# Kernel tuning notes

Hardware: AMD Instinct MI355X
Metric: run time of the kernel (lower is better)

The kernel has to match this reference:

```python
import jax, jax.numpy as jnp
import numpy as np

WH, WW = 16, 16          # window_size
C = 384                  # in_channel
H = 12                   # num_heads
HD = C // H              # head_dim = 32
B = 256                  # num_windows * batch
N = WH * WW              # tokens per window = 256
CPB_HID = 512


def _build_buffers():
    # relative_coords_table: [1, 2*WH-1, 2*WW-1, 2], log-spaced coords (pretrain_window_size = [0,0])
    rch = np.arange(-(WH - 1), WH, dtype=np.float32)
    rcw = np.arange(-(WW - 1), WW, dtype=np.float32)
    table = np.stack(np.meshgrid(rch, rcw, indexing='ij'), axis=-1)[None]  # [1,2WH-1,2WW-1,2]
    table[..., 0] /= (WH - 1)
    table[..., 1] /= (WW - 1)
    table = np.sign(table) * np.log2(np.abs(table) + 1.0) / np.log2(8)
    # relative_position_index: [N, N] int indices into flattened table
    ch = np.arange(WH)
    cw = np.arange(WW)
    coords = np.stack(np.meshgrid(ch, cw, indexing='ij'))      # [2, WH, WW]
    cf = coords.reshape(2, -1)                                  # [2, N]
    rel = cf[:, :, None] - cf[:, None, :]                       # [2, N, N]
    rel = rel.transpose(1, 2, 0).astype(np.int64)               # [N, N, 2]
    rel[..., 0] += WH - 1
    rel[..., 1] += WW - 1
    rel[..., 0] *= 2 * WW - 1
    rpi = rel.sum(-1)                                           # [N, N]
    return jnp.asarray(table, jnp.float32), jnp.asarray(rpi, jnp.int32)


def setup_inputs() -> dict:
    key = jax.random.key(0)
    ks = jax.random.split(key, 9)
    table, rpi = _build_buffers()
    return {
        'x': jax.random.normal(ks[0], (B, N, C), jnp.float32),
        'qkv_w': jax.random.normal(ks[1], (3 * C, C), jnp.float32) * 0.02,
        'q_bias': jnp.zeros((C,), jnp.float32),
        'v_bias': jnp.zeros((C,), jnp.float32),
        'logit_scale': jnp.log(10.0 * jnp.ones((H, 1, 1), jnp.float32)),
        'cpb_w1': jax.random.normal(ks[2], (CPB_HID, 2), jnp.float32) * 0.02,
        'cpb_b1': jnp.zeros((CPB_HID,), jnp.float32),
        'cpb_w2': jax.random.normal(ks[3], (H, CPB_HID), jnp.float32) * 0.02,
        'proj_w': jax.random.normal(ks[4], (C, C), jnp.float32) * 0.02,
        'proj_b': jnp.zeros((C,), jnp.float32),
        'rel_coords_table': table,
        'rel_pos_index': rpi,
    }


def reference(x, qkv_w, q_bias, v_bias, logit_scale, cpb_w1, cpb_b1, cpb_w2,
              proj_w, proj_b, rel_coords_table, rel_pos_index):
    b, n, c = x.shape
    h, hd = H, c // H
    # qkv with q/v bias, zero k bias
    bias = jnp.concatenate([q_bias, jnp.zeros_like(v_bias), v_bias])
    qkv = x @ qkv_w.T + bias                                   # [B,N,3C]
    qkv = qkv.reshape(b, n, 3, h, hd).transpose(2, 0, 3, 1, 4)  # [3,B,H,N,hd]
    q, k, v = qkv[0], qkv[1], qkv[2]
    # cosine attention: L2-normalize q, k (F.normalize with eps=1e-12)
    qn = q / jnp.maximum(jnp.linalg.norm(q, axis=-1, keepdims=True), 1e-12)
    kn = k / jnp.maximum(jnp.linalg.norm(k, axis=-1, keepdims=True), 1e-12)
    attn = jnp.einsum('bhnd,bhmd->bhnm', qn, kn)               # [B,H,N,N]
    # learnable per-head logit scale, clamped at log(1/0.01)
    scale = jnp.exp(jnp.minimum(logit_scale, jnp.log(100.0)))  # [H,1,1]
    attn = attn * scale
    # continuous relative position bias MLP: 2 -> 512 -> H
    hid = jax.nn.relu(rel_coords_table @ cpb_w1.T + cpb_b1)    # [1,2WH-1,2WW-1,512]
    bias_table = (hid @ cpb_w2.T).reshape(-1, h)               # [(2WH-1)*(2WW-1), H]
    rpb = bias_table[rel_pos_index.reshape(-1)].reshape(n, n, h).transpose(2, 0, 1)
    rpb = 16.0 * jax.nn.sigmoid(rpb)                           # [H,N,N]
    attn = jax.nn.softmax(attn + rpb, axis=-1)
    out = jnp.einsum('bhnm,bhmd->bhnd', attn, v)               # [B,H,N,hd]
    out = out.transpose(0, 2, 1, 3).reshape(b, n, c)
    return out @ proj_w.T + proj_b
```

## Files before the change

### kernel.cpp

```cpp
#include <hip/hip_runtime.h>

typedef unsigned int uint;
typedef unsigned short ushort_t;
typedef ushort_t ushort8 __attribute__((ext_vector_type(8)));
typedef ushort_t ushort4v __attribute__((ext_vector_type(4)));
typedef short short8 __attribute__((ext_vector_type(8)));
typedef float floatx4 __attribute__((ext_vector_type(4)));
typedef uint uint2v __attribute__((ext_vector_type(2)));
typedef uint uint4v __attribute__((ext_vector_type(4)));

#define WSQ 25165824L
#define NH  12
#define NT  256
#define HD  32

__device__ __forceinline__ float bf2f(ushort_t u) {
    uint x = ((uint)u) << 16;
    return __builtin_bit_cast(float, x);
}
__device__ __forceinline__ ushort_t f2bf(float f) {
    uint u = __builtin_bit_cast(uint, f);
    uint lsb = (u >> 16) & 1u;
    return (ushort_t)((u + 0x7FFFu + lsb) >> 16);
}
__device__ __forceinline__ uint cvt_pk_bf16(float lo, float hi) {
    uint r;
    asm("v_cvt_pk_bf16_f32 %0, %1, %2" : "=v"(r) : "v"(lo), "v"(hi));
    return r;
}
__device__ __forceinline__ float exp2_fast(float x) {
    float r;
    asm("v_exp_f32 %0, %1" : "=v"(r) : "v"(x));
    return r;
}
__device__ __forceinline__ void permlane32_swap(uint& a, uint& b) {
    uint2v r = __builtin_amdgcn_permlane32_swap(a, b, false, false);
    a = r[0]; b = r[1];
}
__device__ __forceinline__ void permlane16_swap(uint& a, uint& b) {
    uint2v r = __builtin_amdgcn_permlane16_swap(a, b, false, false);
    a = r[0]; b = r[1];
}
__device__ __forceinline__ float ld1(const void* p, long i, int f) {
    return f ? ((const float*)p)[i] : bf2f(((const ushort_t*)p)[i]);
}

__global__ void detect_kernel(const ushort_t* __restrict__ x, int* __restrict__ flag) {
    int t = threadIdx.x;
    uint u = x[2 * t];
    int e = (u >> 7) & 0xFF;
    int weird = (e > 147 || e < 107) ? 1 : 0;
    unsigned long long b = __ballot(weird);
    if (t == 0) *flag = (__popcll(b) > 19) ? 1 : 0;
}

__global__ __launch_bounds__(256) void cvt_kernel(
    const void* __restrict__ src, ushort_t* __restrict__ dst,
    const int* __restrict__ fl, long n8)
{
    long i = (long)blockIdx.x * 256 + threadIdx.x;
    if (i >= n8) return;
    if (*fl) {
        const floatx4* s = (const floatx4*)((const float*)src + i * 8);
        floatx4 a = s[0], b = s[1];
        ushort8 o;
        for (int j = 0; j < 4; ++j) { o[j] = f2bf(a[j]); o[4 + j] = f2bf(b[j]); }
        *(ushort8*)(dst + i * 8) = o;
    } else {
        *(ushort8*)(dst + i * 8) = *(const ushort8*)((const ushort_t*)src + i * 8);
    }
}

__global__ __launch_bounds__(512) void cpb_kernel(
    const void* __restrict__ tab, const void* __restrict__ w1,
    const void* __restrict__ b1, const void* __restrict__ w2,
    const int* __restrict__ fl, float* __restrict__ bt)
{
    __shared__ float hid[512];
    const int f = *fl;
    int p = blockIdx.x, j = threadIdx.x;
    float c0 = ld1(tab, p * 2 + 0, f);
    float c1 = ld1(tab, p * 2 + 1, f);
    float v = ld1(w1, j * 2 + 0, f) * c0 + ld1(w1, j * 2 + 1, f) * c1 + ld1(b1, j, f);
    hid[j] = fmaxf(v, 0.0f);
    __syncthreads();
    if (j < NH) {
        float s = 0.0f;
        for (int i = 0; i < 512; ++i) s += hid[i] * ld1(w2, (long)j * 512 + i, f);
        bt[p * NH + j] = s;
    }
}

__global__ __launch_bounds__(256) void rpb_kernel(
    const int* __restrict__ rpi, const float* __restrict__ bt,
    const void* __restrict__ ls, const int* __restrict__ fl,
    float* __restrict__ rpb)
{
    int idx = blockIdx.x * 256 + threadIdx.x;
    int h = idx >> 16, ij = idx & 65535;
    float x = bt[rpi[ij] * NH + h];
    float scale = __expf(fminf(ld1(ls, h, *fl), 4.6051702f)) * 1.44269504f;
    float bound = fminf(scale, 40.0f) * 1.02f + 23.1f;
    rpb[idx] = 1.44269504f * 16.0f / (1.0f + __expf(-x)) - bound;
}

template <int MODE>
__global__ __launch_bounds__(256) void gemm_bt(
    const ushort_t* __restrict__ A, const ushort_t* __restrict__ Bw,
    const void* __restrict__ bias0, const void* __restrict__ bias2,
    void* __restrict__ Cout, const int* __restrict__ fl)
{
    const int K = 384;
    const int NBX = (MODE == 0) ? 9 : 3;
    const int CHUNK = NBX * 512 / 8;
    __shared__ ushort_t As[128 * 72];
    __shared__ ushort_t Bs[128 * 72];
    const int f = *fl;
    const int tid = threadIdx.x;
    const int w = tid >> 6, lane = tid & 63, l15 = lane & 15, quad = lane >> 4;
    const int bid = blockIdx.x;
    const int wg = (bid & 7) * CHUNK + (bid >> 3);
    const int m0 = (wg / NBX) * 128, n0 = (wg % NBX) * 128;
    const int rw = (w >> 1) * 64, cw = (w & 1) * 64;
    const int lr = tid >> 3, lc = (tid & 7) * 8;

    floatx4 acc[4][4] = {};
    ushort8 pa[4], pb[4];

    for (int i = 0; i < 4; ++i) {
        int r = lr + i * 32;
        if (MODE == 0) {
            pa[i] = *(const ushort8*)&A[(long)(m0 + r) * K + lc];
        } else {
            int m = m0 + r, kc = lc;
            long ad = ((long)(m >> 8) * 12 + (kc >> 5)) * 8192 + (m & 255) * 32 + (kc & 31);
            pa[i] = *(const ushort8*)&A[ad];
        }
        pb[i] = *(const ushort8*)&Bw[(long)(n0 + r) * K + lc];
    }

    for (int kt = 0; kt < K; kt += 64) {
        for (int i = 0; i < 4; ++i) {
            int r = lr + i * 32;
            *(ushort8*)&As[r * 72 + lc] = pa[i];
            *(ushort8*)&Bs[r * 72 + lc] = pb[i];
        }
        __syncthreads();
        if (kt + 64 < K) {
            for (int i = 0; i < 4; ++i) {
                int r = lr + i * 32;
                if (MODE == 0) {
                    pa[i] = *(const ushort8*)&A[(long)(m0 + r) * K + kt + 64 + lc];
                } else {
                    int m = m0 + r, kc = kt + 64 + lc;
                    long ad = ((long)(m >> 8) * 12 + (kc >> 5)) * 8192 + (m & 255) * 32 + (kc & 31);
                    pa[i] = *(const ushort8*)&A[ad];
                }
                pb[i] = *(const ushort8*)&Bw[(long)(n0 + r) * K + kt + 64 + lc];
            }
        }
        for (int ks = 0; ks < 64; ks += 32) {
            short8 af[4], bfr[4];
            for (int mt = 0; mt < 4; ++mt)
                af[mt] = *(short8*)&As[(rw + mt * 16 + l15) * 72 + ks + quad * 8];
            for (int nt = 0; nt < 4; ++nt)
                bfr[nt] = *(short8*)&Bs[(cw + nt * 16 + l15) * 72 + ks + quad * 8];
            for (int mt = 0; mt < 4; ++mt)
                for (int nt = 0; nt < 4; ++nt)
                    acc[mt][nt] = __builtin_amdgcn_mfma_f32_16x16x32_bf16(
                        af[mt], bfr[nt], acc[mt][nt], 0, 0, 0);
        }
        __syncthreads();
    }

    for (int mt = 0; mt < 4; ++mt) {
        for (int nt = 0; nt < 4; ++nt) {
            int c = n0 + cw + nt * 16 + l15;
            if (MODE == 0) {
                int which = c / 384, cc = c % 384;
                float bias = (which == 0) ? ld1(bias0, cc, f)
                           : (which == 2) ? ld1(bias2, cc, f) : 0.0f;
                int hh = cc >> 5, dd = cc & 31;
                for (int r = 0; r < 4; ++r) {
                    int m = m0 + rw + mt * 16 + quad * 4 + r;
                    int b = m >> 8, ntok = m & 255;
                    long dst = (long)which * WSQ +
                               (((long)(b * NH + hh) * NT + ntok) * HD + dd);
                    ((ushort_t*)Cout)[dst] = f2bf(acc[mt][nt][r] + bias);
                }
            } else {
                float bias = ld1(bias0, c, f);
                for (int r = 0; r < 4; ++r) {
                    int m = m0 + rw + mt * 16 + quad * 4 + r;
                    float v = acc[mt][nt][r] + bias;
                    long o = (long)m * 384 + c;
                    if (f) ((float*)Cout)[o] = v;
                    else   ((ushort_t*)Cout)[o] = f2bf(v);
                }
            }
        }
    }
}

__global__ __launch_bounds__(256, 4) void attn_kernel(
    ushort_t* __restrict__ qkv, const void* __restrict__ ls,
    const float* __restrict__ rpb, const int* __restrict__ fl)
{
    __shared__ __attribute__((aligned(16))) ushort_t ks[256 * 40];
    __shared__ __attribute__((aligned(16))) ushort_t vts[32 * 264];

    const int f = *fl;
    const int bid = blockIdx.x;
    const int xcd = bid & 7, local = bid >> 3;
    const int h = local >> 5, bwin = (xcd << 5) + (local & 31);
    const int bh = bwin * NH + h;
    ushort_t* qp = qkv + (long)bh * NT * HD;
    const ushort_t* kp = qp + WSQ;
    const ushort_t* vp = qp + 2 * WSQ;
    const int tid = threadIdx.x;
    const float scale = __expf(fminf(ld1(ls, h, f), 4.6051702f)) * 1.44269504f;

    {
        const int t = tid;
        ushort8 kv[4];
        #pragma unroll
        for (int i = 0; i < 4; ++i) kv[i] = *(const ushort8*)&kp[t * HD + i * 8];
        float fv[32]; float ss = 0.0f;
        #pragma unroll
        for (int i = 0; i < 4; ++i)
            #pragma unroll
            for (int j = 0; j < 8; ++j) {
                float v = bf2f(kv[i][j]); fv[i * 8 + j] = v; ss += v * v;
            }
        float rn = 1.0f / fmaxf(sqrtf(ss), 1e-12f);
        #pragma unroll
        for (int i = 0; i < 4; ++i) {
            uint4v o;
            #pragma unroll
            for (int j = 0; j < 4; ++j)
                o[j] = cvt_pk_bf16(fv[i * 8 + 2 * j] * rn, fv[i * 8 + 2 * j + 1] * rn);
            *(uint4v*)&ks[t * 40 + i * 8] = o;
        }
        ushort8 vv[4];
        #pragma unroll
        for (int i = 0; i < 4; ++i) vv[i] = *(const ushort8*)&vp[t * HD + i * 8];
        #pragma unroll
        for (int i = 0; i < 4; ++i)
            #pragma unroll
            for (int j = 0; j < 8; ++j) vts[(i * 8 + j) * 264 + t] = vv[i][j];
    }
    __syncthreads();

    const int w = tid >> 6, lane = tid & 63, l15 = lane & 15, quad = lane >> 4;

    if (scale <= 40.0f) {
      for (int c = 0; c < 4; ++c) {
        const int mloc = w * 64 + c * 16;

        ushort8 qv = *(const ushort8*)&qp[(mloc + l15) * HD + quad * 8];
        float qf[8]; float ss = 0.0f;
        #pragma unroll
        for (int j = 0; j < 8; ++j) { qf[j] = bf2f(qv[j]); ss += qf[j] * qf[j]; }
        ss += __shfl_xor(ss, 16, 64);
        ss += __shfl_xor(ss, 32, 64);
        float rn = 1.0f / fmaxf(sqrtf(ss), 1e-12f);
        uint4v qa;
        #pragma unroll
        for (int j = 0; j < 4; ++j)
            qa[j] = cvt_pk_bf16(qf[2 * j] * rn, qf[2 * j + 1] * rn);
        short8 aq = __builtin_bit_cast(short8, qa);

        floatx4 accS[16];
        #pragma unroll
        for (int t = 0; t < 16; ++t) {
            short8 bk = *(short8*)&ks[(t * 16 + l15) * 40 + quad * 8];
            floatx4 z = {};
            accS[t] = __builtin_amdgcn_mfma_f32_16x16x32_bf16(bk, aq, z, 0, 0, 0);
        }

        const float* rp = rpb + ((long)h * NT + mloc + l15) * NT;
        const floatx4* rp4 = (const floatx4*)rp;

        float s4[4] = {0.f, 0.f, 0.f, 0.f};
        floatx4 accO[2] = {};
        floatx4 rb0 = rp4[quad], rb1 = rp4[4 + quad];
        #pragma unroll
        for (int kk = 0; kk < 8; ++kk) {
            short8 vf0 = *(short8*)&vts[l15 * 264 + kk * 32 + quad * 8];
            short8 vf1 = *(short8*)&vts[(16 + l15) * 264 + kk * 32 + quad * 8];
            floatx4 nb0 = rb0, nb1 = rb1;
            if (kk < 7) { nb0 = rp4[8 * (kk + 1) + quad]; nb1 = rp4[8 * (kk + 1) + 4 + quad]; }
            const int t0 = 2 * kk, t1 = 2 * kk + 1;
            float a0 = exp2_fast(fmaf(accS[t0][0], scale, rb0[0]));
            float a1 = exp2_fast(fmaf(accS[t0][1], scale, rb0[1]));
            float a2 = exp2_fast(fmaf(accS[t0][2], scale, rb0[2]));
            float a3 = exp2_fast(fmaf(accS[t0][3], scale, rb0[3]));
            float e0 = exp2_fast(fmaf(accS[t1][0], scale, rb1[0]));
            float e1 = exp2_fast(fmaf(accS[t1][1], scale, rb1[1]));
            float e2 = exp2_fast(fmaf(accS[t1][2], scale, rb1[2]));
            float e3 = exp2_fast(fmaf(accS[t1][3], scale, rb1[3]));
            s4[0] += a0 + e0; s4[1] += a1 + e1;
            s4[2] += a2 + e2; s4[3] += a3 + e3;
            uint A0 = cvt_pk_bf16(a0, a1), A1 = cvt_pk_bf16(a2, a3);
            uint B0 = cvt_pk_bf16(e0, e1), B1 = cvt_pk_bf16(e2, e3);
            permlane32_swap(A0, B0); permlane16_swap(A0, B0);
            permlane32_swap(A1, B1); permlane16_swap(A1, B1);
            uint4v pw; pw[0] = A0; pw[1] = A1; pw[2] = B0; pw[3] = B1;
            short8 pf = __builtin_bit_cast(short8, pw);
            accO[0] = __builtin_amdgcn_mfma_f32_16x16x32_bf16(pf, vf0, accO[0], 0, 0, 0);
            accO[1] = __builtin_amdgcn_mfma_f32_16x16x32_bf16(pf, vf1, accO[1], 0, 0, 0);
            rb0 = nb0; rb1 = nb1;
        }

        float rsum = (s4[0] + s4[1]) + (s4[2] + s4[3]);
        rsum += __shfl_xor(rsum, 16, 64);
        rsum += __shfl_xor(rsum, 32, 64);
        float rinv = 1.0f / rsum;
        float ri[4];
        #pragma unroll
        for (int r = 0; r < 4; ++r) ri[r] = __shfl(rinv, quad * 4 + r, 64);

        #pragma unroll
        for (int tn = 0; tn < 2; ++tn)
            #pragma unroll
            for (int r = 0; r < 4; r += 2) {
                uint pk = cvt_pk_bf16(accO[tn][r] * ri[r], accO[tn][r + 1] * ri[r + 1]);
                int n = mloc + quad * 4 + r;
                qp[n * HD + tn * 16 + l15] = (ushort_t)pk;
                qp[(n + 1) * HD + tn * 16 + l15] = (ushort_t)(pk >> 16);
            }
      }
    } else {
      for (int c = 0; c < 4; ++c) {
        const int mloc = w * 64 + c * 16;

        ushort8 qv = *(const ushort8*)&qp[(mloc + l15) * HD + quad * 8];
        float qf[8]; float ss = 0.0f;
        #pragma unroll
        for (int j = 0; j < 8; ++j) { qf[j] = bf2f(qv[j]); ss += qf[j] * qf[j]; }
        ss += __shfl_xor(ss, 16, 64);
        ss += __shfl_xor(ss, 32, 64);
        float rn = 1.0f / fmaxf(sqrtf(ss), 1e-12f);
        uint4v qa;
        #pragma unroll
        for (int j = 0; j < 4; ++j)
            qa[j] = cvt_pk_bf16(qf[2 * j] * rn, qf[2 * j + 1] * rn);
        short8 aq = __builtin_bit_cast(short8, qa);

        floatx4 accS[16];
        #pragma unroll
        for (int t = 0; t < 16; ++t) {
            short8 bk = *(short8*)&ks[(t * 16 + l15) * 40 + quad * 8];
            floatx4 z = {};
            accS[t] = __builtin_amdgcn_mfma_f32_16x16x32_bf16(bk, aq, z, 0, 0, 0);
        }

        const float* rp = rpb + ((long)h * NT + mloc + l15) * NT;
        float m4[4] = {-3e38f, -3e38f, -3e38f, -3e38f};
        #pragma unroll
        for (int t = 0; t < 16; ++t) {
            floatx4 rb = *(const floatx4*)&rp[t * 16 + quad * 4];
            float v0 = fmaf(accS[t][0], scale, rb[0]);
            float v1 = fmaf(accS[t][1], scale, rb[1]);
            float v2 = fmaf(accS[t][2], scale, rb[2]);
            float v3 = fmaf(accS[t][3], scale, rb[3]);
            accS[t][0] = v0; accS[t][1] = v1; accS[t][2] = v2; accS[t][3] = v3;
            m4[t & 3] = fmaxf(m4[t & 3], fmaxf(fmaxf(v0, v1), fmaxf(v2, v3)));
        }
        float rmax = fmaxf(fmaxf(m4[0], m4[1]), fmaxf(m4[2], m4[3]));
        rmax = fmaxf(rmax, __shfl_xor(rmax, 16, 64));
        rmax = fmaxf(rmax, __shfl_xor(rmax, 32, 64));

        float s4[4] = {0.f, 0.f, 0.f, 0.f};
        floatx4 accO[2] = {};
        #pragma unroll
        for (int kk = 0; kk < 8; ++kk) {
            short8 vf0 = *(short8*)&vts[l15 * 264 + kk * 32 + quad * 8];
            short8 vf1 = *(short8*)&vts[(16 + l15) * 264 + kk * 32 + quad * 8];
            const int t0 = 2 * kk, t1 = 2 * kk + 1;
            float a0 = exp2_fast(accS[t0][0] - rmax);
            float a1 = exp2_fast(accS[t0][1] - rmax);
            float a2 = exp2_fast(accS[t0][2] - rmax);
            float a3 = exp2_fast(accS[t0][3] - rmax);
            float e0 = exp2_fast(accS[t1][0] - rmax);
            float e1 = exp2_fast(accS[t1][1] - rmax);
            float e2 = exp2_fast(accS[t1][2] - rmax);
            float e3 = exp2_fast(accS[t1][3] - rmax);
            s4[0] += a0 + e0; s4[1] += a1 + e1;
            s4[2] += a2 + e2; s4[3] += a3 + e3;
            uint A0 = cvt_pk_bf16(a0, a1), A1 = cvt_pk_bf16(a2, a3);
            uint B0 = cvt_pk_bf16(e0, e1), B1 = cvt_pk_bf16(e2, e3);
            permlane32_swap(A0, B0); permlane16_swap(A0, B0);
            permlane32_swap(A1, B1); permlane16_swap(A1, B1);
            uint4v pw; pw[0] = A0; pw[1] = A1; pw[2] = B0; pw[3] = B1;
            short8 pf = __builtin_bit_cast(short8, pw);
            accO[0] = __builtin_amdgcn_mfma_f32_16x16x32_bf16(pf, vf0, accO[0], 0, 0, 0);
            accO[1] = __builtin_amdgcn_mfma_f32_16x16x32_bf16(pf, vf1, accO[1], 0, 0, 0);
        }

        float rsum = (s4[0] + s4[1]) + (s4[2] + s4[3]);
        rsum += __shfl_xor(rsum, 16, 64);
        rsum += __shfl_xor(rsum, 32, 64);
        float rinv = 1.0f / rsum;
        float ri[4];
        #pragma unroll
        for (int r = 0; r < 4; ++r) ri[r] = __shfl(rinv, quad * 4 + r, 64);

        #pragma unroll
        for (int tn = 0; tn < 2; ++tn)
            #pragma unroll
            for (int r = 0; r < 4; r += 2) {
                uint pk = cvt_pk_bf16(accO[tn][r] * ri[r], accO[tn][r + 1] * ri[r + 1]);
                int n = mloc + quad * 4 + r;
                qp[n * HD + tn * 16 + l15] = (ushort_t)pk;
                qp[(n + 1) * HD + tn * 16 + l15] = (ushort_t)(pk >> 16);
            }
      }
    }
}

extern "C" void kernel_launch(void* const* d_in, const int* in_sizes, int n_in,
                              void* d_out, int out_size, void* d_ws, size_t ws_size,
                              hipStream_t stream)
{
    const void* x      = d_in[0];
    const void* qkv_w  = d_in[1];
    const void* q_bias = d_in[2];
    const void* v_bias = d_in[3];
    const void* lscale = d_in[4];
    const void* cpb_w1 = d_in[5];
    const void* cpb_b1 = d_in[6];
    const void* cpb_w2 = d_in[7];
    const void* proj_w = d_in[8];
    const void* proj_b = d_in[9];
    const void* rct    = d_in[10];
    const int*  rpi    = (const int*)d_in[11];

    char* ws = (char*)d_ws;
    ushort_t* qkv_ws  = (ushort_t*)ws;
    float*    bt      = (float*)(ws + 150994944L);
    float*    rpb     = (float*)(ws + 151060480L);
    int*      flag    = (int*)(ws + 154206208L);
    ushort_t* wqkv_b  = (ushort_t*)(ws + 154206464L);
    ushort_t* wproj_b = (ushort_t*)(ws + 155091200L);
    ushort_t* xb      = (ushort_t*)d_out;

    detect_kernel<<<1, 64, 0, stream>>>((const ushort_t*)x, flag);
    cvt_kernel<<<12288, 256, 0, stream>>>(x, xb, flag, 3145728L);
    cvt_kernel<<<216, 256, 0, stream>>>(qkv_w, wqkv_b, flag, 55296L);
    cvt_kernel<<<72, 256, 0, stream>>>(proj_w, wproj_b, flag, 18432L);
    cpb_kernel<<<961, 512, 0, stream>>>(rct, cpb_w1, cpb_b1, cpb_w2, flag, bt);
    rpb_kernel<<<3072, 256, 0, stream>>>(rpi, bt, lscale, flag, rpb);
    gemm_bt<0><<<4608, 256, 0, stream>>>(xb, wqkv_b, q_bias, v_bias, qkv_ws, flag);
    attn_kernel<<<3072, 256, 0, stream>>>(qkv_ws, lscale, rpb, flag);
    gemm_bt<1><<<1536, 256, 0, stream>>>(qkv_ws, wproj_b, proj_b, nullptr, d_out, flag);
}
```

Measured before the change: 468.8 us.

## Fuse fp32-to-bf16 input conversion into GEMM loads and raise MFMA wave priority

```diff
diff --git a/kernel.cpp b/kernel.cpp
--- a/kernel.cpp
+++ b/kernel.cpp
@@ -44,6 +44,17 @@
 __device__ __forceinline__ float ld1(const void* p, long i, int f) {
     return f ? ((const float*)p)[i] : bf2f(((const ushort_t*)p)[i]);
 }
+__device__ __forceinline__ ushort8 ld_bf8(const void* p, long idx, int f) {
+    if (f) {
+        const floatx4* s = (const floatx4*)((const float*)p + idx);
+        floatx4 a = s[0], b = s[1];
+        uint4v u;
+        u[0] = cvt_pk_bf16(a[0], a[1]); u[1] = cvt_pk_bf16(a[2], a[3]);
+        u[2] = cvt_pk_bf16(b[0], b[1]); u[3] = cvt_pk_bf16(b[2], b[3]);
+        return __builtin_bit_cast(ushort8, u);
+    }
+    return *(const ushort8*)((const ushort_t*)p + idx);
+}
 
 __global__ void detect_kernel(const ushort_t* __restrict__ x, int* __restrict__ flag) {
     int t = threadIdx.x;
@@ -52,23 +63,6 @@
     int weird = (e > 147 || e < 107) ? 1 : 0;
     unsigned long long b = __ballot(weird);
     if (t == 0) *flag = (__popcll(b) > 19) ? 1 : 0;
-}
-
-__global__ __launch_bounds__(256) void cvt_kernel(
-    const void* __restrict__ src, ushort_t* __restrict__ dst,
-    const int* __restrict__ fl, long n8)
-{
-    long i = (long)blockIdx.x * 256 + threadIdx.x;
-    if (i >= n8) return;
-    if (*fl) {
-        const floatx4* s = (const floatx4*)((const float*)src + i * 8);
-        floatx4 a = s[0], b = s[1];
-        ushort8 o;
-        for (int j = 0; j < 4; ++j) { o[j] = f2bf(a[j]); o[4 + j] = f2bf(b[j]); }
-        *(ushort8*)(dst + i * 8) = o;
-    } else {
-        *(ushort8*)(dst + i * 8) = *(const ushort8*)((const ushort_t*)src + i * 8);
-    }
 }
 
 __global__ __launch_bounds__(512) void cpb_kernel(
@@ -106,7 +100,7 @@
 
 template <int MODE>
 __global__ __launch_bounds__(256) void gemm_bt(
-    const ushort_t* __restrict__ A, const ushort_t* __restrict__ Bw,
+    const void* __restrict__ A, const void* __restrict__ Bw,
     const void* __restrict__ bias0, const void* __restrict__ bias2,
     void* __restrict__ Cout, const int* __restrict__ fl)
 {
@@ -130,13 +124,13 @@
     for (int i = 0; i < 4; ++i) {
         int r = lr + i * 32;
         if (MODE == 0) {
-            pa[i] = *(const ushort8*)&A[(long)(m0 + r) * K + lc];
+            pa[i] = ld_bf8(A, (long)(m0 + r) * K + lc, f);
         } else {
             int m = m0 + r, kc = lc;
             long ad = ((long)(m >> 8) * 12 + (kc >> 5)) * 8192 + (m & 255) * 32 + (kc & 31);
-            pa[i] = *(const ushort8*)&A[ad];
-        }
-        pb[i] = *(const ushort8*)&Bw[(long)(n0 + r) * K + lc];
+            pa[i] = *(const ushort8*)&((const ushort_t*)A)[ad];
+        }
+        pb[i] = ld_bf8(Bw, (long)(n0 + r) * K + lc, f);
     }
 
     for (int kt = 0; kt < K; kt += 64) {
@@ -150,13 +144,13 @@
             for (int i = 0; i < 4; ++i) {
                 int r = lr + i * 32;
                 if (MODE == 0) {
-                    pa[i] = *(const ushort8*)&A[(long)(m0 + r) * K + kt + 64 + lc];
+                    pa[i] = ld_bf8(A, (long)(m0 + r) * K + kt + 64 + lc, f);
                 } else {
                     int m = m0 + r, kc = kt + 64 + lc;
                     long ad = ((long)(m >> 8) * 12 + (kc >> 5)) * 8192 + (m & 255) * 32 + (kc & 31);
-                    pa[i] = *(const ushort8*)&A[ad];
+                    pa[i] = *(const ushort8*)&((const ushort_t*)A)[ad];
                 }
-                pb[i] = *(const ushort8*)&Bw[(long)(n0 + r) * K + kt + 64 + lc];
+                pb[i] = ld_bf8(Bw, (long)(n0 + r) * K + kt + 64 + lc, f);
             }
         }
         for (int ks = 0; ks < 64; ks += 32) {
@@ -165,10 +159,12 @@
                 af[mt] = *(short8*)&As[(rw + mt * 16 + l15) * 72 + ks + quad * 8];
             for (int nt = 0; nt < 4; ++nt)
                 bfr[nt] = *(short8*)&Bs[(cw + nt * 16 + l15) * 72 + ks + quad * 8];
+            __builtin_amdgcn_s_setprio(1);
             for (int mt = 0; mt < 4; ++mt)
                 for (int nt = 0; nt < 4; ++nt)
                     acc[mt][nt] = __builtin_amdgcn_mfma_f32_16x16x32_bf16(
                         af[mt], bfr[nt], acc[mt][nt], 0, 0, 0);
+            __builtin_amdgcn_s_setprio(0);
         }
         __syncthreads();
     }
@@ -271,12 +267,14 @@
         short8 aq = __builtin_bit_cast(short8, qa);
 
         floatx4 accS[16];
+        __builtin_amdgcn_s_setprio(1);
         #pragma unroll
         for (int t = 0; t < 16; ++t) {
             short8 bk = *(short8*)&ks[(t * 16 + l15) * 40 + quad * 8];
             floatx4 z = {};
             accS[t] = __builtin_amdgcn_mfma_f32_16x16x32_bf16(bk, aq, z, 0, 0, 0);
         }
+        __builtin_amdgcn_s_setprio(0);
 
         const float* rp = rpb + ((long)h * NT + mloc + l15) * NT;
         const floatx4* rp4 = (const floatx4*)rp;
@@ -307,8 +305,10 @@
             permlane32_swap(A1, B1); permlane16_swap(A1, B1);
             uint4v pw; pw[0] = A0; pw[1] = A1; pw[2] = B0; pw[3] = B1;
             short8 pf = __builtin_bit_cast(short8, pw);
+            __builtin_amdgcn_s_setprio(1);
             accO[0] = __builtin_amdgcn_mfma_f32_16x16x32_bf16(pf, vf0, accO[0], 0, 0, 0);
             accO[1] = __builtin_amdgcn_mfma_f32_16x16x32_bf16(pf, vf1, accO[1], 0, 0, 0);
+            __builtin_amdgcn_s_setprio(0);
             rb0 = nb0; rb1 = nb1;
         }
 
@@ -441,17 +441,11 @@
     float*    bt      = (float*)(ws + 150994944L);
     float*    rpb     = (float*)(ws + 151060480L);
     int*      flag    = (int*)(ws + 154206208L);
-    ushort_t* wqkv_b  = (ushort_t*)(ws + 154206464L);
-    ushort_t* wproj_b = (ushort_t*)(ws + 155091200L);
-    ushort_t* xb      = (ushort_t*)d_out;
 
     detect_kernel<<<1, 64, 0, stream>>>((const ushort_t*)x, flag);
-    cvt_kernel<<<12288, 256, 0, stream>>>(x, xb, flag, 3145728L);
-    cvt_kernel<<<216, 256, 0, stream>>>(qkv_w, wqkv_b, flag, 55296L);
-    cvt_kernel<<<72, 256, 0, stream>>>(proj_w, wproj_b, flag, 18432L);
     cpb_kernel<<<961, 512, 0, stream>>>(rct, cpb_w1, cpb_b1, cpb_w2, flag, bt);
     rpb_kernel<<<3072, 256, 0, stream>>>(rpi, bt, lscale, flag, rpb);
-    gemm_bt<0><<<4608, 256, 0, stream>>>(xb, wqkv_b, q_bias, v_bias, qkv_ws, flag);
+    gemm_bt<0><<<4608, 256, 0, stream>>>(x, qkv_w, q_bias, v_bias, qkv_ws, flag);
     attn_kernel<<<3072, 256, 0, stream>>>(qkv_ws, lscale, rpb, flag);
-    gemm_bt<1><<<1536, 256, 0, stream>>>(qkv_ws, wproj_b, proj_b, nullptr, d_out, flag);
-}
+    gemm_bt<1><<<1536, 256, 0, stream>>>(qkv_ws, proj_w, proj_b, nullptr, d_out, flag);
+}
```

Measured after the change: 621.5 us. 32.6% more time.

## Use direct global-to-LDS loads with XOR swizzle in GEMM, add MFMA priority hints

Applied to the files above, without the earlier changes.

```diff
diff --git a/kernel.cpp b/kernel.cpp
--- a/kernel.cpp
+++ b/kernel.cpp
@@ -44,6 +44,11 @@
 __device__ __forceinline__ float ld1(const void* p, long i, int f) {
     return f ? ((const float*)p)[i] : bf2f(((const ushort_t*)p)[i]);
 }
+__device__ __forceinline__ void gld_lds16(const ushort_t* g, ushort_t* l) {
+    __builtin_amdgcn_global_load_lds(
+        (const __attribute__((address_space(1))) void*)g,
+        (__attribute__((address_space(3))) void*)l, 16, 0, 0);
+}
 
 __global__ void detect_kernel(const ushort_t* __restrict__ x, int* __restrict__ flag) {
     int t = threadIdx.x;
@@ -63,9 +68,10 @@
     if (*fl) {
         const floatx4* s = (const floatx4*)((const float*)src + i * 8);
         floatx4 a = s[0], b = s[1];
-        ushort8 o;
-        for (int j = 0; j < 4; ++j) { o[j] = f2bf(a[j]); o[4 + j] = f2bf(b[j]); }
-        *(ushort8*)(dst + i * 8) = o;
+        uint4v u;
+        u[0] = cvt_pk_bf16(a[0], a[1]); u[1] = cvt_pk_bf16(a[2], a[3]);
+        u[2] = cvt_pk_bf16(b[0], b[1]); u[3] = cvt_pk_bf16(b[2], b[3]);
+        *(uint4v*)(dst + i * 8) = u;
     } else {
         *(ushort8*)(dst + i * 8) = *(const ushort8*)((const ushort_t*)src + i * 8);
     }
@@ -113,8 +119,8 @@
     const int K = 384;
     const int NBX = (MODE == 0) ? 9 : 3;
     const int CHUNK = NBX * 512 / 8;
-    __shared__ ushort_t As[128 * 72];
-    __shared__ ushort_t Bs[128 * 72];
+    __shared__ __attribute__((aligned(16))) ushort_t As[128 * 64];
+    __shared__ __attribute__((aligned(16))) ushort_t Bs[128 * 64];
     const int f = *fl;
     const int tid = threadIdx.x;
     const int w = tid >> 6, lane = tid & 63, l15 = lane & 15, quad = lane >> 4;
@@ -122,55 +128,48 @@
     const int wg = (bid & 7) * CHUNK + (bid >> 3);
     const int m0 = (wg / NBX) * 128, n0 = (wg % NBX) * 128;
     const int rw = (w >> 1) * 64, cw = (w & 1) * 64;
-    const int lr = tid >> 3, lc = (tid & 7) * 8;
+
+    const int lrow = lane >> 3;
+    const int lcs  = ((lane & 7) ^ lrow) * 8;
+    const int sw   = (l15 & 7) * 8;
 
     floatx4 acc[4][4] = {};
-    ushort8 pa[4], pb[4];
-
-    for (int i = 0; i < 4; ++i) {
-        int r = lr + i * 32;
-        if (MODE == 0) {
-            pa[i] = *(const ushort8*)&A[(long)(m0 + r) * K + lc];
-        } else {
-            int m = m0 + r, kc = lc;
-            long ad = ((long)(m >> 8) * 12 + (kc >> 5)) * 8192 + (m & 255) * 32 + (kc & 31);
-            pa[i] = *(const ushort8*)&A[ad];
-        }
-        pb[i] = *(const ushort8*)&Bw[(long)(n0 + r) * K + lc];
-    }
 
     for (int kt = 0; kt < K; kt += 64) {
-        for (int i = 0; i < 4; ++i) {
-            int r = lr + i * 32;
-            *(ushort8*)&As[r * 72 + lc] = pa[i];
-            *(ushort8*)&Bs[r * 72 + lc] = pb[i];
+        if (kt) __syncthreads();
+        #pragma unroll
+        for (int j = 0; j < 4; ++j) {
+            const int c = w * 4 + j;
+            const int row = c * 8 + lrow;
+            long ga;
+            if (MODE == 0) {
+                ga = (long)(m0 + row) * K + kt + lcs;
+            } else {
+                int m = m0 + row, kc = kt + lcs;
+                ga = ((long)(m >> 8) * 12 + (kc >> 5)) * 8192 + (m & 255) * 32 + (kc & 31);
+            }
+            gld_lds16(&A[ga], &As[c * 512]);
+            long gb = (long)(n0 + row) * K + kt + lcs;
+            gld_lds16(&Bw[gb], &Bs[c * 512]);
         }
         __syncthreads();
-        if (kt + 64 < K) {
-            for (int i = 0; i < 4; ++i) {
-                int r = lr + i * 32;
-                if (MODE == 0) {
-                    pa[i] = *(const ushort8*)&A[(long)(m0 + r) * K + kt + 64 + lc];
-                } else {
-                    int m = m0 + r, kc = kt + 64 + lc;
-                    long ad = ((long)(m >> 8) * 12 + (kc >> 5)) * 8192 + (m & 255) * 32 + (kc & 31);
-                    pa[i] = *(const ushort8*)&A[ad];
-                }
-                pb[i] = *(const ushort8*)&Bw[(long)(n0 + r) * K + kt + 64 + lc];
-            }
-        }
+        #pragma unroll
         for (int ks = 0; ks < 64; ks += 32) {
             short8 af[4], bfr[4];
+            const int col = (ks + quad * 8) ^ sw;
+            #pragma unroll
             for (int mt = 0; mt < 4; ++mt)
-                af[mt] = *(short8*)&As[(rw + mt * 16 + l15) * 72 + ks + quad * 8];
+                af[mt] = *(short8*)&As[(rw + mt * 16 + l15) * 64 + col];
+            #pragma unroll
             for (int nt = 0; nt < 4; ++nt)
-                bfr[nt] = *(short8*)&Bs[(cw + nt * 16 + l15) * 72 + ks + quad * 8];
+                bfr[nt] = *(short8*)&Bs[(cw + nt * 16 + l15) * 64 + col];
+            #pragma unroll
             for (int mt = 0; mt < 4; ++mt)
+                #pragma unroll
                 for (int nt = 0; nt < 4; ++nt)
                     acc[mt][nt] = __builtin_amdgcn_mfma_f32_16x16x32_bf16(
                         af[mt], bfr[nt], acc[mt][nt], 0, 0, 0);
         }
-        __syncthreads();
     }
 
     for (int mt = 0; mt < 4; ++mt) {
@@ -271,12 +270,14 @@
         short8 aq = __builtin_bit_cast(short8, qa);
 
         floatx4 accS[16];
+        __builtin_amdgcn_s_setprio(1);
         #pragma unroll
         for (int t = 0; t < 16; ++t) {
             short8 bk = *(short8*)&ks[(t * 16 + l15) * 40 + quad * 8];
             floatx4 z = {};
             accS[t] = __builtin_amdgcn_mfma_f32_16x16x32_bf16(bk, aq, z, 0, 0, 0);
         }
+        __builtin_amdgcn_s_setprio(0);
 
         const float* rp = rpb + ((long)h * NT + mloc + l15) * NT;
         const floatx4* rp4 = (const floatx4*)rp;
@@ -307,8 +308,10 @@
             permlane32_swap(A1, B1); permlane16_swap(A1, B1);
             uint4v pw; pw[0] = A0; pw[1] = A1; pw[2] = B0; pw[3] = B1;
             short8 pf = __builtin_bit_cast(short8, pw);
+            __builtin_amdgcn_s_setprio(1);
             accO[0] = __builtin_amdgcn_mfma_f32_16x16x32_bf16(pf, vf0, accO[0], 0, 0, 0);
             accO[1] = __builtin_amdgcn_mfma_f32_16x16x32_bf16(pf, vf1, accO[1], 0, 0, 0);
+            __builtin_amdgcn_s_setprio(0);
             rb0 = nb0; rb1 = nb1;
         }
 
```

Result: no change. 468.7 us (-0.0%).
